# Optimization experiments

Measured on AMD Instinct MI355X. Metric: run time of the kernel, lower is better.

The kernel has to match this reference:

```python
import jax, jax.numpy as jnp
import numpy as np

NUM_HEADS = 16
EMBED_DIM = 1024
HEAD_DIM = EMBED_DIM // NUM_HEADS  # 64


def setup_inputs() -> dict:
    key = jax.random.key(0)
    k1, k2, k3 = jax.random.split(key, 3)
    x = jax.random.normal(k1, (2, 2048, EMBED_DIM), dtype=jnp.float32)
    # torch Linear(head_dim, 3*head_dim): weight [3*hd, hd], bias [3*hd]
    # stored here as W_qkv [hd, 3*hd] so that y = x @ W_qkv + b
    lim = 1.0 / np.sqrt(HEAD_DIM)
    W_qkv = jax.random.uniform(k2, (HEAD_DIM, 3 * HEAD_DIM), minval=-lim, maxval=lim, dtype=jnp.float32)
    b_qkv = jax.random.uniform(k3, (3 * HEAD_DIM,), minval=-lim, maxval=lim, dtype=jnp.float32)
    return {"x": x, "W_qkv": W_qkv, "b_qkv": b_qkv}


def reference(x, W_qkv, b_qkv):
    B, T, E = x.shape
    # [B, T, E] -> [B, H, T, hd]
    xh = x.reshape(B, T, NUM_HEADS, HEAD_DIM).transpose(0, 2, 1, 3)
    qkv = xh @ W_qkv + b_qkv  # [B, H, T, 3*hd], shared weights across heads
    q, k, v = jnp.split(qkv, 3, axis=-1)
    scale = 1.0 / jnp.sqrt(jnp.asarray(HEAD_DIM, dtype=x.dtype))
    scores = jnp.einsum('bhqd,bhkd->bhqk', q, k) * scale  # [B, H, T, T]
    attn = jax.nn.softmax(scores, axis=-1)
    out = jnp.einsum('bhqk,bhkd->bhqd', attn, v)  # [B, H, T, hd]
    return out.transpose(0, 2, 1, 3).reshape(B, T, E)
```

## Files before the change

kernel.cpp:

```cpp
#include <hip/hip_runtime.h>
#include <hip/hip_bf16.h>

#define T_SEQ   2048
#define EMBED   1024
#define HD      64
#define NHEADS  16
#define NBH     32
#define QSCALE  0.18033688011112042f

typedef __attribute__((ext_vector_type(8))) short short8;
typedef __attribute__((ext_vector_type(4))) float f32x4;
typedef __attribute__((ext_vector_type(2))) unsigned int uint2v;
typedef __attribute__((ext_vector_type(4))) unsigned int uint4v;

#if __has_builtin(__builtin_amdgcn_exp2f)
#define EXP2F __builtin_amdgcn_exp2f
#else
#define EXP2F exp2f
#endif

__device__ __forceinline__ ushort bf16r(float f) {
  union { float f; unsigned u; } v; v.f = f;
  return (ushort)((v.u + 0x8000u) >> 16);
}

__device__ __forceinline__ unsigned pk2bf_perm(float a, float b) {
  union { float f; unsigned u; } ua, ub; ua.f = a; ub.f = b;
  return __builtin_amdgcn_perm(ub.u + 0x8000u, ua.u + 0x8000u, 0x07060302u);
}
#if __has_builtin(__builtin_amdgcn_cvt_pk_bf16_f32)
typedef __attribute__((ext_vector_type(2))) __bf16 bf16x2;
__device__ __forceinline__ unsigned pkbf(float a, float b) {
  union { bf16x2 v; unsigned u; } c;
  c.v = __builtin_amdgcn_cvt_pk_bf16_f32(a, b);
  return c.u;
}
#else
#define pkbf pk2bf_perm
#endif

__device__ __forceinline__ uint2v pl32swap(unsigned a, unsigned b) {
#if __has_builtin(__builtin_amdgcn_permlane32_swap)
  return __builtin_amdgcn_permlane32_swap(a, b, false, false);
#else
  asm("v_permlane32_swap_b32 %0, %1" : "+v"(a), "+v"(b));
  return (uint2v){a, b};
#endif
}
__device__ __forceinline__ uint2v pl16swap(unsigned a, unsigned b) {
#if __has_builtin(__builtin_amdgcn_permlane16_swap)
  return __builtin_amdgcn_permlane16_swap(a, b, false, false);
#else
  asm("v_permlane16_swap_b32 %0, %1" : "+v"(a), "+v"(b));
  return (uint2v){a, b};
#endif
}

__device__ __forceinline__ void async16(const ushort* g, ushort* l) {
  __builtin_amdgcn_global_load_lds(
      (const __attribute__((address_space(1))) unsigned int*)g,
      (__attribute__((address_space(3))) unsigned int*)l, 16, 0, 0);
}

__global__ __launch_bounds__(256) void prep_w(const float* __restrict__ W,
                                              ushort* __restrict__ Wg) {
  const int i = blockIdx.x * 256 + threadIdx.x;
  const int d = i / 192, c = i - d * 192;
  const int phys = c * 64 + (((d >> 3) ^ (c & 7)) << 3) + (d & 7);
  Wg[phys] = bf16r(W[i]);
}

__global__ __launch_bounds__(256) void qkv_proj(
    const float* __restrict__ x, const ushort* __restrict__ Wg,
    const float* __restrict__ bias,
    ushort* __restrict__ Qws, ushort* __restrict__ Kws,
    ushort* __restrict__ Vtws) {
  __shared__ ushort WtL[192 * 64];
  __shared__ float bl[192];

  const int bx = blockIdx.x;
  const int b  = bx >> 9;
  const int h  = (bx >> 5) & 15;
  const int t0 = (bx & 31) * 64;
  const int tid = threadIdx.x;
  const int wave = tid >> 6, lane = tid & 63;
  const int quad = lane >> 4, n16 = lane & 15;

  const int trow = t0 + wave * 16 + n16;
  const float* xr = x + ((size_t)(b * T_SEQ + trow)) * EMBED + h * HD;
  short8 xa[2];
#pragma unroll
  for (int ks = 0; ks < 2; ks++) {
    f32x4 v0 = *(const f32x4*)(xr + ks * 32 + quad * 8);
    f32x4 v1 = *(const f32x4*)(xr + ks * 32 + quad * 8 + 4);
    short8 f;
    ((unsigned*)&f)[0] = pkbf(v0[0], v0[1]);
    ((unsigned*)&f)[1] = pkbf(v0[2], v0[3]);
    ((unsigned*)&f)[2] = pkbf(v1[0], v1[1]);
    ((unsigned*)&f)[3] = pkbf(v1[2], v1[3]);
    xa[ks] = f;
  }

#pragma unroll
  for (int it = 0; it < 6; it++)
    async16(Wg + it * 2048 + tid * 8, WtL + it * 2048 + wave * 512);
  if (tid < 192) bl[tid] = bias[tid];
  __syncthreads();

  const int bh = b * NHEADS + h;
  const size_t qkbase = (size_t)bh * T_SEQ * HD;
  const int tw = t0 + wave * 16;
  const int sw = n16 & 7;

#pragma unroll
  for (int nt = 0; nt < 12; nt++) {
    const ushort* wrow = WtL + (nt * 16 + n16) * 64;
    const short8 wb0 = *(short8*)(wrow + ((quad ^ sw) << 3));
    const short8 wb1 = *(short8*)(wrow + (((4 | quad) ^ sw) << 3));
    const float bv = bl[nt * 16 + n16];
    f32x4 acc = (f32x4){0.f, 0.f, 0.f, 0.f};
    acc = __builtin_amdgcn_mfma_f32_16x16x32_bf16(xa[0], wb0, acc, 0, 0, 0);
    acc = __builtin_amdgcn_mfma_f32_16x16x32_bf16(xa[1], wb1, acc, 0, 0, 0);
    if (nt < 4) {
      const int d = nt * 16 + n16;
#pragma unroll
      for (int r = 0; r < 4; r++)
        Qws[qkbase + (size_t)(tw + quad * 4 + r) * HD + d] =
            bf16r((acc[r] + bv) * QSCALE);
    } else if (nt < 8) {
      const int d = (nt - 4) * 16 + n16;
#pragma unroll
      for (int r = 0; r < 4; r++)
        Kws[qkbase + (size_t)(tw + quad * 4 + r) * HD + d] =
            bf16r(acc[r] + bv);
    } else {
      const int d = (nt - 8) * 16 + n16;
      const int tcol = tw + quad * 4;
      uint2v pk;
      pk.x = pkbf(acc[0] + bv, acc[1] + bv);
      pk.y = pkbf(acc[2] + bv, acc[3] + bv);
      *(uint2v*)(Vtws + (size_t)(bh * HD + d) * T_SEQ + tcol) = pk;
    }
  }
}

__global__ __launch_bounds__(256) void flash_attn(
    const ushort* __restrict__ Qws, const ushort* __restrict__ Kws,
    const ushort* __restrict__ Vtws, float* __restrict__ out) {
  __shared__ ushort Ks[2][64 * 64];
  __shared__ ushort Vs[2][64 * 64];

  const int bx = blockIdx.x;
  const int bh = bx & 31;
  const int q0 = (bx >> 5) * 128;
  const int b = bh >> 4, h = bh & 15;
  const int tid = threadIdx.x;
  const int wave = tid >> 6, lane = tid & 63;
  const int quad = lane >> 4, n16 = lane & 15;

  const ushort* Qb = Qws + (size_t)bh * T_SEQ * HD;
  const ushort* Kb = Kws + (size_t)bh * T_SEQ * HD;
  const ushort* Vb = Vtws + (size_t)bh * HD * T_SEQ;

  short8 qa[2][2];
#pragma unroll
  for (int hf = 0; hf < 2; hf++)
#pragma unroll
    for (int ks = 0; ks < 2; ks++) {
      const int row = q0 + wave * 32 + hf * 16 + n16;
      qa[hf][ks] = *(const short8*)(Qb + (size_t)row * HD + ks * 32 + quad * 8);
    }

  const int sr = tid >> 3, sp = tid & 7;
  const int sl = (sp ^ (sr & 7)) * 8;
  const ushort* srcK0 = Kb + (size_t)sr * HD + sl;
  const ushort* srcK1 = Kb + (size_t)(sr + 32) * HD + sl;
  const ushort* srcV0 = Vb + (size_t)sr * T_SEQ + sl;
  const ushort* srcV1 = Vb + (size_t)(sr + 32) * T_SEQ + sl;

  int foff[2];
#pragma unroll
  for (int ks = 0; ks < 2; ks++)
    foff[ks] = n16 * 64 + ((((ks << 2) | quad) ^ (n16 & 7)) << 3);

  f32x4 o[2][4];
  float ls[2] = {0.f, 0.f};
#pragma unroll
  for (int hf = 0; hf < 2; hf++)
#pragma unroll
    for (int nt = 0; nt < 4; nt++) o[hf][nt] = (f32x4){0.f, 0.f, 0.f, 0.f};

  async16(srcK0, Ks[0] + wave * 512);
  async16(srcK1, Ks[0] + 2048 + wave * 512);
  async16(srcV0, Vs[0] + wave * 512);
  async16(srcV1, Vs[0] + 2048 + wave * 512);
  __syncthreads();

  for (int kt = 0; kt < 32; kt++) {
    const int bsel = kt & 1;
    if (kt < 31) {
      const size_t kK = (size_t)(kt + 1) * 64 * HD;
      const size_t kV = (size_t)(kt + 1) * 64;
      async16(srcK0 + kK, Ks[bsel ^ 1] + wave * 512);
      async16(srcK1 + kK, Ks[bsel ^ 1] + 2048 + wave * 512);
      async16(srcV0 + kV, Vs[bsel ^ 1] + wave * 512);
      async16(srcV1 + kV, Vs[bsel ^ 1] + 2048 + wave * 512);
    }
    const ushort* Kt = Ks[bsel];
    const ushort* Vt = Vs[bsel];

    f32x4 s0[4], s1[4];
#pragma unroll
    for (int nt = 0; nt < 4; nt++) {
      const short8 ka0 = *(short8*)(Kt + (nt << 10) + foff[0]);
      const short8 ka1 = *(short8*)(Kt + (nt << 10) + foff[1]);
      f32x4 a0 = (f32x4){0.f, 0.f, 0.f, 0.f};
      f32x4 a1 = (f32x4){0.f, 0.f, 0.f, 0.f};
      a0 = __builtin_amdgcn_mfma_f32_16x16x32_bf16(ka0, qa[0][0], a0, 0, 0, 0);
      a0 = __builtin_amdgcn_mfma_f32_16x16x32_bf16(ka1, qa[0][1], a0, 0, 0, 0);
      a1 = __builtin_amdgcn_mfma_f32_16x16x32_bf16(ka0, qa[1][0], a1, 0, 0, 0);
      a1 = __builtin_amdgcn_mfma_f32_16x16x32_bf16(ka1, qa[1][1], a1, 0, 0, 0);
      s0[nt] = a0;
      s1[nt] = a1;
    }

    short8 pa[2][2];
#pragma unroll
    for (int hf = 0; hf < 2; hf++) {
      unsigned P01[4], P23[4];
      float lacc = 0.f;
#pragma unroll
      for (int nt = 0; nt < 4; nt++) {
        const f32x4 sv = hf ? s1[nt] : s0[nt];
        float p0 = EXP2F(sv[0]), p1 = EXP2F(sv[1]);
        float p2 = EXP2F(sv[2]), p3 = EXP2F(sv[3]);
        lacc += (p0 + p1) + (p2 + p3);
        P01[nt] = pkbf(p0, p1);
        P23[nt] = pkbf(p2, p3);
      }
      ls[hf] += lacc;
#pragma unroll
      for (int ks = 0; ks < 2; ks++) {
        uint2v tA = pl32swap(P01[2 * ks], P01[2 * ks + 1]);
        uint2v uA = pl16swap(tA.x, tA.y);
        uint2v tB = pl32swap(P23[2 * ks], P23[2 * ks + 1]);
        uint2v uB = pl16swap(tB.x, tB.y);
        union { uint4v u; short8 s; } c;
        c.u = (uint4v){uA.x, uB.x, uA.y, uB.y};
        pa[hf][ks] = c.s;
      }
    }

#pragma unroll
    for (int nt = 0; nt < 4; nt++) {
      const short8 vb0 = *(short8*)(Vt + (nt << 10) + foff[0]);
      const short8 vb1 = *(short8*)(Vt + (nt << 10) + foff[1]);
      o[0][nt] = __builtin_amdgcn_mfma_f32_16x16x32_bf16(pa[0][0], vb0, o[0][nt], 0, 0, 0);
      o[0][nt] = __builtin_amdgcn_mfma_f32_16x16x32_bf16(pa[0][1], vb1, o[0][nt], 0, 0, 0);
      o[1][nt] = __builtin_amdgcn_mfma_f32_16x16x32_bf16(pa[1][0], vb0, o[1][nt], 0, 0, 0);
      o[1][nt] = __builtin_amdgcn_mfma_f32_16x16x32_bf16(pa[1][1], vb1, o[1][nt], 0, 0, 0);
    }
    __syncthreads();
  }

#pragma unroll
  for (int hf = 0; hf < 2; hf++) {
    ls[hf] += __shfl_xor(ls[hf], 16, 64);
    ls[hf] += __shfl_xor(ls[hf], 32, 64);
  }

#pragma unroll
  for (int hf = 0; hf < 2; hf++) {
#pragma unroll
    for (int r = 0; r < 4; r++) {
      const float rl = 1.0f / __shfl(ls[hf], quad * 4 + r, 64);
      const int row = q0 + wave * 32 + hf * 16 + quad * 4 + r;
#pragma unroll
      for (int nt = 0; nt < 4; nt++) {
        const int d = nt * 16 + n16;
        out[(size_t)(b * T_SEQ + row) * EMBED + h * HD + d] = o[hf][nt][r] * rl;
      }
    }
  }
}

extern "C" void kernel_launch(void* const* d_in, const int* in_sizes, int n_in,
                              void* d_out, int out_size, void* d_ws, size_t ws_size,
                              hipStream_t stream) {
  (void)in_sizes; (void)n_in; (void)out_size; (void)ws_size;
  const float* x    = (const float*)d_in[0];
  const float* W    = (const float*)d_in[1];
  const float* bias = (const float*)d_in[2];
  float* out = (float*)d_out;

  const size_t elems = (size_t)NBH * T_SEQ * HD;
  ushort* Qws  = (ushort*)d_ws;
  ushort* Kws  = Qws + elems;
  ushort* Vtws = Kws + elems;
  ushort* Wg   = Vtws + elems;

  prep_w<<<dim3(48), dim3(256), 0, stream>>>(W, Wg);
  qkv_proj<<<dim3(1024), dim3(256), 0, stream>>>(x, Wg, bias, Qws, Kws, Vtws);
  flash_attn<<<dim3(512), dim3(256), 0, stream>>>(Qws, Kws, Vtws, out);
}
```

Measured before the change: 133.7 us.

## Triple-buffer K/V loads, use one barrier per tile, compute row sums via MFMA

Grows the K/V shared-memory ring from two buffers to four and prefetches two tiles ahead. The single trailing __syncthreads is replaced by an explicit vmcnt wait plus s_barrier at the top of each iteration, so global loads get more time in flight. The softmax denominator is now accumulated with extra MFMAs against a vector of bf16 ones instead of scalar adds and cross-lane shuffles. s_setprio is raised around the MFMA sections. This doubles LDS use per block, which may lower occupancy, and the row sums now come from bf16-rounded probabilities.

```diff
diff --git a/kernel.cpp b/kernel.cpp
--- a/kernel.cpp
+++ b/kernel.cpp
@@ -147,8 +147,8 @@
 __global__ __launch_bounds__(256) void flash_attn(
     const ushort* __restrict__ Qws, const ushort* __restrict__ Kws,
     const ushort* __restrict__ Vtws, float* __restrict__ out) {
-  __shared__ ushort Ks[2][64 * 64];
-  __shared__ ushort Vs[2][64 * 64];
+  __shared__ ushort Ks[4][64 * 64];
+  __shared__ ushort Vs[4][64 * 64];
 
   const int bx = blockIdx.x;
   const int bh = bx & 31;
@@ -183,33 +183,51 @@
   for (int ks = 0; ks < 2; ks++)
     foff[ks] = n16 * 64 + ((((ks << 2) | quad) ^ (n16 & 7)) << 3);
 
+  short8 ones;
+#pragma unroll
+  for (int j = 0; j < 8; j++) ones[j] = (short)0x3F80;
+
   f32x4 o[2][4];
-  float ls[2] = {0.f, 0.f};
-#pragma unroll
-  for (int hf = 0; hf < 2; hf++)
+  f32x4 lA[2];
+#pragma unroll
+  for (int hf = 0; hf < 2; hf++) {
+    lA[hf] = (f32x4){0.f, 0.f, 0.f, 0.f};
 #pragma unroll
     for (int nt = 0; nt < 4; nt++) o[hf][nt] = (f32x4){0.f, 0.f, 0.f, 0.f};
+  }
 
   async16(srcK0, Ks[0] + wave * 512);
   async16(srcK1, Ks[0] + 2048 + wave * 512);
   async16(srcV0, Vs[0] + wave * 512);
   async16(srcV1, Vs[0] + 2048 + wave * 512);
-  __syncthreads();
+  async16(srcK0 + 64 * HD, Ks[1] + wave * 512);
+  async16(srcK1 + 64 * HD, Ks[1] + 2048 + wave * 512);
+  async16(srcV0 + 64, Vs[1] + wave * 512);
+  async16(srcV1 + 64, Vs[1] + 2048 + wave * 512);
 
   for (int kt = 0; kt < 32; kt++) {
-    const int bsel = kt & 1;
-    if (kt < 31) {
-      const size_t kK = (size_t)(kt + 1) * 64 * HD;
-      const size_t kV = (size_t)(kt + 1) * 64;
-      async16(srcK0 + kK, Ks[bsel ^ 1] + wave * 512);
-      async16(srcK1 + kK, Ks[bsel ^ 1] + 2048 + wave * 512);
-      async16(srcV0 + kV, Vs[bsel ^ 1] + wave * 512);
-      async16(srcV1 + kV, Vs[bsel ^ 1] + 2048 + wave * 512);
-    }
-    const ushort* Kt = Ks[bsel];
-    const ushort* Vt = Vs[bsel];
+    const int cb = kt & 3;
+    if (kt < 30) {
+      const int pb = (kt + 2) & 3;
+      const size_t kK = (size_t)(kt + 2) * 64 * HD;
+      const size_t kV = (size_t)(kt + 2) * 64;
+      async16(srcK0 + kK, Ks[pb] + wave * 512);
+      async16(srcK1 + kK, Ks[pb] + 2048 + wave * 512);
+      async16(srcV0 + kV, Vs[pb] + wave * 512);
+      async16(srcV1 + kV, Vs[pb] + 2048 + wave * 512);
+    }
+    __builtin_amdgcn_sched_barrier(0);
+    if (kt < 30)       asm volatile("s_waitcnt vmcnt(8)" ::: "memory");
+    else if (kt == 30) asm volatile("s_waitcnt vmcnt(4)" ::: "memory");
+    else               asm volatile("s_waitcnt vmcnt(0)" ::: "memory");
+    __builtin_amdgcn_s_barrier();
+    __builtin_amdgcn_sched_barrier(0);
+
+    const ushort* Kt = Ks[cb];
+    const ushort* Vt = Vs[cb];
 
     f32x4 s0[4], s1[4];
+    __builtin_amdgcn_s_setprio(1);
 #pragma unroll
     for (int nt = 0; nt < 4; nt++) {
       const short8 ka0 = *(short8*)(Kt + (nt << 10) + foff[0]);
@@ -223,22 +241,20 @@
       s0[nt] = a0;
       s1[nt] = a1;
     }
+    __builtin_amdgcn_s_setprio(0);
 
     short8 pa[2][2];
 #pragma unroll
     for (int hf = 0; hf < 2; hf++) {
       unsigned P01[4], P23[4];
-      float lacc = 0.f;
 #pragma unroll
       for (int nt = 0; nt < 4; nt++) {
         const f32x4 sv = hf ? s1[nt] : s0[nt];
         float p0 = EXP2F(sv[0]), p1 = EXP2F(sv[1]);
         float p2 = EXP2F(sv[2]), p3 = EXP2F(sv[3]);
-        lacc += (p0 + p1) + (p2 + p3);
         P01[nt] = pkbf(p0, p1);
         P23[nt] = pkbf(p2, p3);
       }
-      ls[hf] += lacc;
 #pragma unroll
       for (int ks = 0; ks < 2; ks++) {
         uint2v tA = pl32swap(P01[2 * ks], P01[2 * ks + 1]);
@@ -251,6 +267,7 @@
       }
     }
 
+    __builtin_amdgcn_s_setprio(1);
 #pragma unroll
     for (int nt = 0; nt < 4; nt++) {
       const short8 vb0 = *(short8*)(Vt + (nt << 10) + foff[0]);
@@ -260,20 +277,19 @@
       o[1][nt] = __builtin_amdgcn_mfma_f32_16x16x32_bf16(pa[1][0], vb0, o[1][nt], 0, 0, 0);
       o[1][nt] = __builtin_amdgcn_mfma_f32_16x16x32_bf16(pa[1][1], vb1, o[1][nt], 0, 0, 0);
     }
-    __syncthreads();
+#pragma unroll
+    for (int hf = 0; hf < 2; hf++) {
+      lA[hf] = __builtin_amdgcn_mfma_f32_16x16x32_bf16(pa[hf][0], ones, lA[hf], 0, 0, 0);
+      lA[hf] = __builtin_amdgcn_mfma_f32_16x16x32_bf16(pa[hf][1], ones, lA[hf], 0, 0, 0);
+    }
+    __builtin_amdgcn_s_setprio(0);
   }
 
 #pragma unroll
   for (int hf = 0; hf < 2; hf++) {
-    ls[hf] += __shfl_xor(ls[hf], 16, 64);
-    ls[hf] += __shfl_xor(ls[hf], 32, 64);
-  }
-
-#pragma unroll
-  for (int hf = 0; hf < 2; hf++) {
 #pragma unroll
     for (int r = 0; r < 4; r++) {
-      const float rl = 1.0f / __shfl(ls[hf], quad * 4 + r, 64);
+      const float rl = 1.0f / lA[hf][r];
       const int row = q0 + wave * 32 + hf * 16 + quad * 4 + r;
 #pragma unroll
       for (int nt = 0; nt < 4; nt++) {
```

Measured after the change: 123.7 us. 7.5% less time.
